# Optimization experiments

Measured on AMD Instinct MI355X. Metric: run time of the kernel, lower is better.

Reference implementation:

```python
import jax, jax.numpy as jnp
import numpy as np

H, C = 3, 64  # heads, per-head channels
NEG_SLOPE = 0.2

def setup_inputs() -> dict:
    key = jax.random.key(0)
    ks = jax.random.split(key, 8)
    B, N, D, E = 2, 50000, 128, 800000
    h = jax.random.normal(ks[0], (B, N, D), dtype=jnp.float32)
    edge_index = jax.random.randint(ks[1], (2, E), 0, N, dtype=jnp.int64)
    s = 1.0 / np.sqrt(D)
    W = jax.random.normal(ks[2], (D, H * C), dtype=jnp.float32) * s
    a_src = jax.random.normal(ks[3], (H, C), dtype=jnp.float32) * (1.0 / np.sqrt(C))
    a_dst = jax.random.normal(ks[4], (H, C), dtype=jnp.float32) * (1.0 / np.sqrt(C))
    bias = jnp.zeros((H * C,), dtype=jnp.float32)
    Wo = jax.random.normal(ks[5], (H * C, 1), dtype=jnp.float32) * (1.0 / np.sqrt(H * C))
    bo = jnp.zeros((1,), dtype=jnp.float32)
    return {"h": h, "edge_index": edge_index, "W": W, "a_src": a_src,
            "a_dst": a_dst, "bias": bias, "Wo": Wo, "bo": bo}

def _gat_single(h_b, src, dst, N, W, a_src, a_dst, bias):
    # h_b: [N, D] -> x: [N, H, C]
    x = (h_b @ W).reshape(-1, H, C)
    alpha_s = jnp.einsum('nhc,hc->nh', x, a_src)  # [N, H]
    alpha_d = jnp.einsum('nhc,hc->nh', x, a_dst)  # [N, H]
    e = alpha_s[src] + alpha_d[dst]               # [E', H]
    e = jnp.where(e > 0, e, NEG_SLOPE * e)        # leaky_relu(0.2)
    # segment softmax over edges grouped by destination node
    emax = jax.ops.segment_max(e, dst, num_segments=N)          # [N, H]
    p = jnp.exp(e - emax[dst])
    denom = jax.ops.segment_sum(p, dst, num_segments=N)         # [N, H]
    att = p / (denom[dst] + 1e-16)                               # [E', H]
    out = jax.ops.segment_sum(att[:, :, None] * x[src], dst, num_segments=N)  # [N,H,C]
    return out.reshape(-1, H * C) + bias

def reference(h, edge_index, W, a_src, a_dst, bias, Wo, bo):
    B, N, D = h.shape
    # PyG GATConv default: add self loops
    loops = jnp.arange(N, dtype=edge_index.dtype)
    src = jnp.concatenate([edge_index[0], loops])
    dst = jnp.concatenate([edge_index[1], loops])
    gat = jax.vmap(lambda hb: _gat_single(hb, src, dst, N, W, a_src, a_dst, bias))(h)
    gat = jax.nn.elu(gat)            # [B, N, H*C]; dropout inactive (eval)
    logits = gat @ Wo + bo           # [B, N, 1]
    return logits
```

## Files before the change

kernel.cpp:

```cpp
#include <hip/hip_runtime.h>
#include <hip/hip_bf16.h>
#include <math.h>

typedef __hip_bfloat16 bf16;
typedef __attribute__((ext_vector_type(8))) short short8;
typedef __attribute__((ext_vector_type(4))) float f32x4;

#define HC 192
#define DIN 128
#define NEG_SLOPE 0.2f
#define LCH 128
#define GN 4

static inline int cdiv(int a, int b){ return (a + b - 1) / b; }

__device__ inline short f2bf(float f){
  __hip_bfloat16 b = __float2bfloat16(f);
  return __builtin_bit_cast(short, b);
}
__device__ inline float loadf(const void* p, size_t i, int fm){
  return fm ? __bfloat162float(((const bf16*)p)[i]) : ((const float*)p)[i];
}
__device__ inline int eload(const void* p, long long i, int em){
  return em ? (int)(((const long long*)p)[i]) : ((const int*)p)[i];
}
__device__ inline unsigned pack2h(float a, float b){
  unsigned short ha = __builtin_bit_cast(unsigned short, (_Float16)a);
  unsigned short hb = __builtin_bit_cast(unsigned short, (_Float16)b);
  return (unsigned)ha | ((unsigned)hb << 16);
}
__device__ inline float unph(unsigned w, int hi){
  unsigned short hs = hi ? (unsigned short)(w >> 16) : (unsigned short)(w & 0xffff);
  return (float)__builtin_bit_cast(_Float16, hs);
}

__device__ inline int detect_fm(const unsigned* __restrict__ hw){
  unsigned w = hw[threadIdx.x & 63];
  unsigned expo = (w >> 7) & 0xFF;
  unsigned long long m = __ballot(expo >= 100 && expo <= 135);
  return __popcll(m) > 32;
}
__device__ inline int detect_em(const unsigned* __restrict__ ew){
  unsigned long long m = __ballot(ew[2*(threadIdx.x & 63) + 1] != 0);
  return __popcll(m) < 32;
}

__global__ void k_repack(const void* __restrict__ W, const void* __restrict__ a_src,
    const void* __restrict__ a_dst, const void* __restrict__ bias,
    const void* __restrict__ Wo, const void* __restrict__ bo,
    const unsigned* __restrict__ hw, bf16* __restrict__ Wt,
    float* __restrict__ asf, float* __restrict__ adf, float* __restrict__ biasf,
    float* __restrict__ Wof, float* __restrict__ bof){
  int fm = detect_fm(hw);
  int idx = blockIdx.x * 256 + threadIdx.x;
  if (idx < DIN * HC){
    int d = idx / HC, j = idx - d * HC;
    Wt[j * DIN + d] = __float2bfloat16(loadf(W, idx, fm));
  }
  if (idx < HC){
    asf[idx]   = loadf(a_src, idx, fm);
    adf[idx]   = loadf(a_dst, idx, fm);
    biasf[idx] = loadf(bias, idx, fm);
    Wof[idx]   = loadf(Wo, idx, fm);
  }
  if (idx == 0) bof[0] = loadf(bo, 0, fm);
}

__global__ __launch_bounds__(256) void k_gemm(const void* __restrict__ h,
    const bf16* __restrict__ Wt, bf16* __restrict__ x,
    const float* __restrict__ asf, const float* __restrict__ adf,
    float* __restrict__ asp, float* __restrict__ adp, int M, int N){
  int fm   = detect_fm((const unsigned*)h);
  int tid  = threadIdx.x;
  int w    = tid >> 6;
  int lane = tid & 63;
  int r16  = lane & 15;
  int quad = lane >> 4;
  __shared__ short ldsW[HC * 136];
  for (int c = tid; c < HC * 16; c += 256){
    int row = c >> 4, kg = c & 15;
    *(short8*)&ldsW[row * 136 + kg * 8] = *(const short8*)(Wt + row * DIN + kg * 8);
  }
  __syncthreads();

  int row  = blockIdx.x * 64 + w * 16 + r16;
  int lrow = min(row, M - 1);
  f32x4 acc[12];
  #pragma unroll
  for (int i = 0; i < 12; i++) acc[i] = (f32x4){0.f,0.f,0.f,0.f};
  size_t abase = (size_t)lrow * DIN + quad * 8;
  #pragma unroll
  for (int kb = 0; kb < 4; kb++){
    short8 af;
    if (fm == 0){
      const float* hf = (const float*)h + abase + kb * 32;
      float4 a = *(const float4*)hf;
      float4 b = *(const float4*)(hf + 4);
      af[0]=f2bf(a.x); af[1]=f2bf(a.y); af[2]=f2bf(a.z); af[3]=f2bf(a.w);
      af[4]=f2bf(b.x); af[5]=f2bf(b.y); af[6]=f2bf(b.z); af[7]=f2bf(b.w);
    } else {
      af = *(const short8*)((const bf16*)h + abase + kb * 32);
    }
    #pragma unroll
    for (int nt = 0; nt < 12; nt++){
      short8 bf_ = *(const short8*)&ldsW[(nt*16 + r16) * 136 + kb * 32 + quad * 8];
      acc[nt] = __builtin_amdgcn_mfma_f32_16x16x32_bf16(af, bf_, acc[nt], 0,0,0);
    }
  }
  int rbase = blockIdx.x * 64 + w * 16 + quad * 4;
  #pragma unroll
  for (int nt = 0; nt < 12; nt++){
    #pragma unroll
    for (int r = 0; r < 4; r++){
      int rr = rbase + r;
      if (rr < M) x[(size_t)rr * HC + nt*16 + r16] = __float2bfloat16(acc[nt][r]);
    }
  }
  float asv[12], adv[12];
  #pragma unroll
  for (int nt = 0; nt < 12; nt++){
    int col = (nt >> 2) * 64 + (nt & 3) * 16 + r16;
    asv[nt] = asf[col];
    adv[nt] = adf[col];
  }
  #pragma unroll
  for (int hh = 0; hh < 3; hh++){
    #pragma unroll
    for (int r = 0; r < 4; r++){
      float vs = acc[4*hh+0][r]*asv[4*hh+0] + acc[4*hh+1][r]*asv[4*hh+1]
               + acc[4*hh+2][r]*asv[4*hh+2] + acc[4*hh+3][r]*asv[4*hh+3];
      float vd = acc[4*hh+0][r]*adv[4*hh+0] + acc[4*hh+1][r]*adv[4*hh+1]
               + acc[4*hh+2][r]*adv[4*hh+2] + acc[4*hh+3][r]*adv[4*hh+3];
      #pragma unroll
      for (int off = 8; off; off >>= 1){
        vs += __shfl_down(vs, off, 16);
        vd += __shfl_down(vd, off, 16);
      }
      if (r16 == 0){
        int rr = rbase + r;
        if (rr < M){
          int b = rr >= N;
          int node = rr - b * N;
          asp[(size_t)node*8 + b*3 + hh] = vs;
          adp[(size_t)node*8 + b*3 + hh] = vd;
        }
      }
    }
  }
}

__global__ void k_hist(const void* __restrict__ ei, int E, int N, int* counts){
  int em = detect_em((const unsigned*)ei);
  int idx = blockIdx.x * 256 + threadIdx.x;
  if (idx >= E + N) return;
  int d = (idx < E) ? eload(ei, (long long)E + idx, em) : (idx - E);
  if ((unsigned)d < (unsigned)N) atomicAdd(&counts[d], 1);
}

__global__ __launch_bounds__(256) void k_scanA(const int* __restrict__ counts,
    int* __restrict__ partial, int* __restrict__ bsums, int N){
  __shared__ int s[256];
  int t = threadIdx.x, idx = blockIdx.x * 256 + t;
  int v = (idx < N) ? counts[idx] : 0;
  s[t] = v; __syncthreads();
  for (int o = 1; o < 256; o <<= 1){
    int u = (t >= o) ? s[t - o] : 0;
    __syncthreads();
    s[t] += u;
    __syncthreads();
  }
  if (idx < N) partial[idx] = s[t] - v;
  if (t == 255) bsums[blockIdx.x] = s[255];
}

__global__ __launch_bounds__(256) void k_scanC(const int* __restrict__ partial,
    const int* __restrict__ bsums, int* __restrict__ row_ptr,
    int* __restrict__ cursor, int N, int nb){
  __shared__ int s[256];
  int t = threadIdx.x;
  int v = (t < nb) ? bsums[t] : 0;
  s[t] = v; __syncthreads();
  for (int o = 1; o < 256; o <<= 1){
    int u = (t >= o) ? s[t - o] : 0;
    __syncthreads();
    s[t] += u;
    __syncthreads();
  }
  int excl = s[t] - v;
  __syncthreads();
  s[t] = excl;
  __syncthreads();
  int idx = blockIdx.x * 256 + t;
  int boff = s[blockIdx.x];
  if (idx < N){
    int val = partial[idx] + boff;
    row_ptr[idx] = val;
    cursor[idx]  = val;
  } else if (idx == N){
    row_ptr[N] = s[nb-1] + bsums[nb-1];
  }
}

__global__ void k_scatter(const void* __restrict__ ei, int E, int N,
    int* cursor, int2* __restrict__ esd){
  int em = detect_em((const unsigned*)ei);
  int idx = blockIdx.x * 256 + threadIdx.x;
  if (idx >= E + N) return;
  int s, d;
  if (idx < E){
    s = eload(ei, idx, em);
    d = eload(ei, (long long)E + idx, em);
  } else { s = d = idx - E; }
  if ((unsigned)d >= (unsigned)N) return;
  if ((unsigned)s >= (unsigned)N) s = 0;
  int p = atomicAdd(&cursor[d], 1);
  esd[p] = make_int2(s, d);
}

__global__ __launch_bounds__(256) void k_pe(const int2* __restrict__ esd,
    const float* __restrict__ asp, const float* __restrict__ adp,
    uint4* __restrict__ pe, int Etot){
  int j = blockIdx.x * 256 + threadIdx.x;
  if (j >= Etot) return;
  int2 sd = esd[j];
  float4 A0 = ((const float4*)asp)[(size_t)sd.x*2];
  float4 A1 = ((const float4*)asp)[(size_t)sd.x*2 + 1];
  float4 D0 = ((const float4*)adp)[(size_t)sd.y*2];
  float4 D1 = ((const float4*)adp)[(size_t)sd.y*2 + 1];
  float e0 = A0.x + D0.x, e1 = A0.y + D0.y, e2 = A0.z + D0.z;
  float e3 = A0.w + D0.w, e4 = A1.x + D1.x, e5 = A1.y + D1.y;
  e0 = e0 > 0.f ? e0 : NEG_SLOPE*e0;  e1 = e1 > 0.f ? e1 : NEG_SLOPE*e1;
  e2 = e2 > 0.f ? e2 : NEG_SLOPE*e2;  e3 = e3 > 0.f ? e3 : NEG_SLOPE*e3;
  e4 = e4 > 0.f ? e4 : NEG_SLOPE*e4;  e5 = e5 > 0.f ? e5 : NEG_SLOPE*e5;
  uint4 rec;
  rec.x = pack2h(__expf(e0), __expf(e1));
  rec.y = pack2h(__expf(e2), __expf(e3));
  rec.z = pack2h(__expf(e4), __expf(e5));
  rec.w = (unsigned)sd.x;
  pe[j] = rec;
}

__global__ __launch_bounds__(192) void k_gat(const bf16* __restrict__ x,
    const uint4* __restrict__ pe, const int* __restrict__ row_ptr,
    const float* __restrict__ biasf, const float* __restrict__ Wof,
    const float* __restrict__ bof, float* __restrict__ out, int N){
  int blk  = blockIdx.x;
  int t    = threadIdx.x;
  int node = t / 48;
  int u    = t - node * 48;
  int b    = u >= 24;
  int c8   = u - b * 24;
  int hh   = c8 >> 3;
  __shared__ int   rp[GN + 1];
  __shared__ uint4 ldsR[LCH];
  __shared__ float red[192];
  if (t < GN + 1) rp[t] = row_ptr[GN*blk + t];
  __syncthreads();
  int start = rp[node], end = rp[node + 1];
  int base0 = rp[0], cend = rp[GN];
  const ushort* xb = (const ushort*)x + (size_t)b * N * HC + c8 * 8;
  int pidx = b*3 + hh;
  int pw_i = pidx >> 1, pw_h = pidx & 1;
  unsigned* ldsU = (unsigned*)ldsR;
  float acc[8];
  #pragma unroll
  for (int k = 0; k < 8; k++) acc[k] = 0.f;
  float den = 0.f;
  for (int cb = base0; cb < cend; cb += LCH){
    int cnt = min(LCH, cend - cb);
    __syncthreads();
    for (int j = t; j < cnt; j += 192) ldsR[j] = pe[(size_t)cb + j];
    __syncthreads();
    int i0 = max(start, cb), i1 = min(end, cb + cnt);
    #pragma unroll 4
    for (int i = i0; i < i1; i++){
      int rec = i - cb;
      float p = unph(ldsU[rec*4 + pw_i], pw_h);
      int s   = (int)ldsU[rec*4 + 3];
      uint4 q = *(const uint4*)(xb + (size_t)s * HC);
      den += p;
      acc[0] = fmaf(p, __uint_as_float(q.x << 16),         acc[0]);
      acc[1] = fmaf(p, __uint_as_float(q.x & 0xffff0000u), acc[1]);
      acc[2] = fmaf(p, __uint_as_float(q.y << 16),         acc[2]);
      acc[3] = fmaf(p, __uint_as_float(q.y & 0xffff0000u), acc[3]);
      acc[4] = fmaf(p, __uint_as_float(q.z << 16),         acc[4]);
      acc[5] = fmaf(p, __uint_as_float(q.z & 0xffff0000u), acc[5]);
      acc[6] = fmaf(p, __uint_as_float(q.w << 16),         acc[6]);
      acc[7] = fmaf(p, __uint_as_float(q.w & 0xffff0000u), acc[7]);
    }
  }
  float inv = 1.f / (den + 1e-16f);
  float4 bi0 = ((const float4*)biasf)[c8*2], bi1 = ((const float4*)biasf)[c8*2+1];
  float4 w0  = ((const float4*)Wof)[c8*2],  w1  = ((const float4*)Wof)[c8*2+1];
  float r = 0.f;
  {
    float v;
    v = acc[0]*inv + bi0.x; v = v > 0.f ? v : expm1f(v); r += v * w0.x;
    v = acc[1]*inv + bi0.y; v = v > 0.f ? v : expm1f(v); r += v * w0.y;
    v = acc[2]*inv + bi0.z; v = v > 0.f ? v : expm1f(v); r += v * w0.z;
    v = acc[3]*inv + bi0.w; v = v > 0.f ? v : expm1f(v); r += v * w0.w;
    v = acc[4]*inv + bi1.x; v = v > 0.f ? v : expm1f(v); r += v * w1.x;
    v = acc[5]*inv + bi1.y; v = v > 0.f ? v : expm1f(v); r += v * w1.y;
    v = acc[6]*inv + bi1.z; v = v > 0.f ? v : expm1f(v); r += v * w1.z;
    v = acc[7]*inv + bi1.w; v = v > 0.f ? v : expm1f(v); r += v * w1.w;
  }
  red[t] = r;
  __syncthreads();
  if (t < 64){
    int g = t >> 3, l = t & 7;
    float v = red[g*24 + l] + red[g*24 + 8 + l] + red[g*24 + 16 + l];
    v += __shfl_down(v, 4, 8);
    v += __shfl_down(v, 2, 8);
    v += __shfl_down(v, 1, 8);
    if (l == 0){
      int nd = GN*blk + (g >> 1);
      int bb = g & 1;
      out[(size_t)bb * N + nd] = v + bof[0];
    }
  }
}

extern "C" void kernel_launch(void* const* d_in, const int* in_sizes, int n_in,
                              void* d_out, int out_size, void* d_ws, size_t ws_size,
                              hipStream_t stream){
  const void* h     = d_in[0];
  const void* ei    = d_in[1];
  const void* W     = d_in[2];
  const void* a_src = d_in[3];
  const void* a_dst = d_in[4];
  const void* bias  = d_in[5];
  const void* Wo    = d_in[6];
  const void* bo    = d_in[7];
  float* out = (float*)d_out;

  const int M    = in_sizes[0] / DIN;
  const int N    = M / 2;
  const int E    = in_sizes[1] / 2;
  const int Etot = E + N;

  char* ws = (char*)d_ws;
  size_t off = 0;
  auto alloc = [&](size_t bytes) -> void* {
    void* p = ws + off;
    off = (off + bytes + 511) & ~(size_t)511;
    return p;
  };
  bf16*  x       = (bf16*) alloc((size_t)M * HC * sizeof(bf16));
  float* asp     = (float*)alloc((size_t)N * 8 * sizeof(float));
  float* adp     = (float*)alloc((size_t)N * 8 * sizeof(float));
  int*   counts  = (int*)  alloc((size_t)N * sizeof(int));
  int*   partial = (int*)  alloc((size_t)N * sizeof(int));
  int*   row_ptr = (int*)  alloc((size_t)(N + 1) * sizeof(int));
  int*   cursor  = (int*)  alloc((size_t)N * sizeof(int));
  int*   bsums   = (int*)  alloc(256 * sizeof(int));
  int2*  esd     = (int2*) alloc((size_t)Etot * sizeof(int2));
  uint4* pe      = (uint4*)alloc((size_t)Etot * sizeof(uint4));
  bf16*  Wt      = (bf16*) alloc((size_t)DIN * HC * sizeof(bf16));
  float* asf     = (float*)alloc(HC * sizeof(float));
  float* adf     = (float*)alloc(HC * sizeof(float));
  float* biasf   = (float*)alloc(HC * sizeof(float));
  float* Wof     = (float*)alloc(HC * sizeof(float));
  float* bof     = (float*)alloc(16 * sizeof(float));
  (void)ws_size; (void)n_in; (void)out_size;

  hipMemsetAsync(counts, 0, (size_t)N * sizeof(int), stream);

  k_repack<<<cdiv(DIN * HC, 256), 256, 0, stream>>>(W, a_src, a_dst, bias, Wo, bo,
      (const unsigned*)h, Wt, asf, adf, biasf, Wof, bof);
  k_gemm<<<cdiv(M, 64), 256, 0, stream>>>(h, Wt, x, asf, adf, asp, adp, M, N);
  k_hist<<<cdiv(Etot, 256), 256, 0, stream>>>(ei, E, N, counts);
  int nb = cdiv(N, 256);
  k_scanA<<<nb, 256, 0, stream>>>(counts, partial, bsums, N);
  k_scanC<<<cdiv(N + 1, 256), 256, 0, stream>>>(partial, bsums, row_ptr, cursor, N, nb);
  k_scatter<<<cdiv(Etot, 256), 256, 0, stream>>>(ei, E, N, cursor, esd);
  k_pe<<<cdiv(Etot, 256), 256, 0, stream>>>(esd, asp, adp, pe, Etot);
  k_gat<<<N / GN, 192, 0, stream>>>(x, pe, row_ptr, biasf, Wof, bof, out, N);
}
```

Measured before the change: 315.1 us.

## Fuse CSR build and edge precompute into one persistent kernel with grid barriers

Replaces the histogram, two scan kernels, scatter and per-edge exp kernels with a single persistent kernel of 256 blocks that uses software grid barriers between phases. The scatter phase now computes the packed attention exponentials directly and writes them to the CSR slot, which removes the intermediate src/dst buffer and its extra write and read pass. This cuts four kernel launches and one global round trip. In exchange it relies on all 256 blocks being co-resident for the spin barriers, and it runs the edge loops with fewer threads using grid-stride loops. The single-block scan of block sums assumes at most 256 blocks, which fits N=50000.

```diff
diff --git a/kernel.cpp b/kernel.cpp
--- a/kernel.cpp
+++ b/kernel.cpp
@@ -11,6 +11,7 @@
 #define NEG_SLOPE 0.2f
 #define LCH 128
 #define GN 4
+#define CSRG 256
 
 static inline int cdiv(int a, int b){ return (a + b - 1) / b; }
 
@@ -43,6 +44,17 @@
 __device__ inline int detect_em(const unsigned* __restrict__ ew){
   unsigned long long m = __ballot(ew[2*(threadIdx.x & 63) + 1] != 0);
   return __popcll(m) < 32;
+}
+
+__device__ inline void gbar(int* bar, int id){
+  __syncthreads();
+  if (threadIdx.x == 0){
+    __threadfence();
+    __hip_atomic_fetch_add(&bar[id], 1, __ATOMIC_RELEASE, __HIP_MEMORY_SCOPE_AGENT);
+    while (__hip_atomic_load(&bar[id], __ATOMIC_ACQUIRE, __HIP_MEMORY_SCOPE_AGENT) < CSRG) {}
+    __threadfence();
+  }
+  __syncthreads();
 }
 
 __global__ void k_repack(const void* __restrict__ W, const void* __restrict__ a_src,
@@ -149,19 +161,24 @@
   }
 }
 
-__global__ void k_hist(const void* __restrict__ ei, int E, int N, int* counts){
+__global__ __launch_bounds__(256) void k_csr(const void* __restrict__ ei,
+    int E, int N, int* __restrict__ counts, int* __restrict__ bar,
+    int* __restrict__ partial, int* __restrict__ bsums,
+    int* __restrict__ row_ptr, int* __restrict__ cursor,
+    const float* __restrict__ asp, const float* __restrict__ adp,
+    uint4* __restrict__ pe){
   int em = detect_em((const unsigned*)ei);
-  int idx = blockIdx.x * 256 + threadIdx.x;
-  if (idx >= E + N) return;
-  int d = (idx < E) ? eload(ei, (long long)E + idx, em) : (idx - E);
-  if ((unsigned)d < (unsigned)N) atomicAdd(&counts[d], 1);
-}
-
-__global__ __launch_bounds__(256) void k_scanA(const int* __restrict__ counts,
-    int* __restrict__ partial, int* __restrict__ bsums, int N){
+  int t = threadIdx.x, blk = blockIdx.x;
+  int gt = blk * 256 + t;
+  const int GT = CSRG * 256;
+  int Etot = E + N;
+  for (int idx = gt; idx < Etot; idx += GT){
+    int d = (idx < E) ? eload(ei, (long long)E + idx, em) : (idx - E);
+    if ((unsigned)d < (unsigned)N) atomicAdd(&counts[d], 1);
+  }
+  gbar(bar, 0);
   __shared__ int s[256];
-  int t = threadIdx.x, idx = blockIdx.x * 256 + t;
-  int v = (idx < N) ? counts[idx] : 0;
+  int v = (gt < N) ? counts[gt] : 0;
   s[t] = v; __syncthreads();
   for (int o = 1; o < 256; o <<= 1){
     int u = (t >= o) ? s[t - o] : 0;
@@ -169,75 +186,52 @@
     s[t] += u;
     __syncthreads();
   }
-  if (idx < N) partial[idx] = s[t] - v;
-  if (t == 255) bsums[blockIdx.x] = s[255];
-}
-
-__global__ __launch_bounds__(256) void k_scanC(const int* __restrict__ partial,
-    const int* __restrict__ bsums, int* __restrict__ row_ptr,
-    int* __restrict__ cursor, int N, int nb){
-  __shared__ int s[256];
-  int t = threadIdx.x;
-  int v = (t < nb) ? bsums[t] : 0;
-  s[t] = v; __syncthreads();
+  if (gt < N) partial[gt] = s[t] - v;
+  if (t == 255) bsums[blk] = s[255];
+  gbar(bar, 1);
+  int v2 = bsums[t];
+  s[t] = v2; __syncthreads();
   for (int o = 1; o < 256; o <<= 1){
     int u = (t >= o) ? s[t - o] : 0;
     __syncthreads();
     s[t] += u;
     __syncthreads();
   }
-  int excl = s[t] - v;
-  __syncthreads();
-  s[t] = excl;
-  __syncthreads();
-  int idx = blockIdx.x * 256 + t;
-  int boff = s[blockIdx.x];
-  if (idx < N){
-    int val = partial[idx] + boff;
-    row_ptr[idx] = val;
-    cursor[idx]  = val;
-  } else if (idx == N){
-    row_ptr[N] = s[nb-1] + bsums[nb-1];
-  }
-}
-
-__global__ void k_scatter(const void* __restrict__ ei, int E, int N,
-    int* cursor, int2* __restrict__ esd){
-  int em = detect_em((const unsigned*)ei);
-  int idx = blockIdx.x * 256 + threadIdx.x;
-  if (idx >= E + N) return;
-  int s, d;
-  if (idx < E){
-    s = eload(ei, idx, em);
-    d = eload(ei, (long long)E + idx, em);
-  } else { s = d = idx - E; }
-  if ((unsigned)d >= (unsigned)N) return;
-  if ((unsigned)s >= (unsigned)N) s = 0;
-  int p = atomicAdd(&cursor[d], 1);
-  esd[p] = make_int2(s, d);
-}
-
-__global__ __launch_bounds__(256) void k_pe(const int2* __restrict__ esd,
-    const float* __restrict__ asp, const float* __restrict__ adp,
-    uint4* __restrict__ pe, int Etot){
-  int j = blockIdx.x * 256 + threadIdx.x;
-  if (j >= Etot) return;
-  int2 sd = esd[j];
-  float4 A0 = ((const float4*)asp)[(size_t)sd.x*2];
-  float4 A1 = ((const float4*)asp)[(size_t)sd.x*2 + 1];
-  float4 D0 = ((const float4*)adp)[(size_t)sd.y*2];
-  float4 D1 = ((const float4*)adp)[(size_t)sd.y*2 + 1];
-  float e0 = A0.x + D0.x, e1 = A0.y + D0.y, e2 = A0.z + D0.z;
-  float e3 = A0.w + D0.w, e4 = A1.x + D1.x, e5 = A1.y + D1.y;
-  e0 = e0 > 0.f ? e0 : NEG_SLOPE*e0;  e1 = e1 > 0.f ? e1 : NEG_SLOPE*e1;
-  e2 = e2 > 0.f ? e2 : NEG_SLOPE*e2;  e3 = e3 > 0.f ? e3 : NEG_SLOPE*e3;
-  e4 = e4 > 0.f ? e4 : NEG_SLOPE*e4;  e5 = e5 > 0.f ? e5 : NEG_SLOPE*e5;
-  uint4 rec;
-  rec.x = pack2h(__expf(e0), __expf(e1));
-  rec.y = pack2h(__expf(e2), __expf(e3));
-  rec.z = pack2h(__expf(e4), __expf(e5));
-  rec.w = (unsigned)sd.x;
-  pe[j] = rec;
+  int total = s[255];
+  int boff  = s[blk] - bsums[blk];
+  if (gt < N){
+    int val = partial[gt] + boff;
+    row_ptr[gt] = val;
+    cursor[gt]  = val;
+  } else if (gt == N){
+    row_ptr[N] = total;
+  }
+  gbar(bar, 2);
+  for (int idx = gt; idx < Etot; idx += GT){
+    int sn, d;
+    if (idx < E){
+      sn = eload(ei, idx, em);
+      d  = eload(ei, (long long)E + idx, em);
+    } else { sn = d = idx - E; }
+    if ((unsigned)d >= (unsigned)N) continue;
+    if ((unsigned)sn >= (unsigned)N) sn = 0;
+    int p = atomicAdd(&cursor[d], 1);
+    float4 A0 = ((const float4*)asp)[(size_t)sn*2];
+    float4 A1 = ((const float4*)asp)[(size_t)sn*2 + 1];
+    float4 D0 = ((const float4*)adp)[(size_t)d*2];
+    float4 D1 = ((const float4*)adp)[(size_t)d*2 + 1];
+    float e0 = A0.x + D0.x, e1 = A0.y + D0.y, e2 = A0.z + D0.z;
+    float e3 = A0.w + D0.w, e4 = A1.x + D1.x, e5 = A1.y + D1.y;
+    e0 = e0 > 0.f ? e0 : NEG_SLOPE*e0;  e1 = e1 > 0.f ? e1 : NEG_SLOPE*e1;
+    e2 = e2 > 0.f ? e2 : NEG_SLOPE*e2;  e3 = e3 > 0.f ? e3 : NEG_SLOPE*e3;
+    e4 = e4 > 0.f ? e4 : NEG_SLOPE*e4;  e5 = e5 > 0.f ? e5 : NEG_SLOPE*e5;
+    uint4 rec;
+    rec.x = pack2h(__expf(e0), __expf(e1));
+    rec.y = pack2h(__expf(e2), __expf(e3));
+    rec.z = pack2h(__expf(e4), __expf(e5));
+    rec.w = (unsigned)sn;
+    pe[p] = rec;
+  }
 }
 
 __global__ __launch_bounds__(192) void k_gat(const bf16* __restrict__ x,
@@ -348,12 +342,12 @@
   bf16*  x       = (bf16*) alloc((size_t)M * HC * sizeof(bf16));
   float* asp     = (float*)alloc((size_t)N * 8 * sizeof(float));
   float* adp     = (float*)alloc((size_t)N * 8 * sizeof(float));
-  int*   counts  = (int*)  alloc((size_t)N * sizeof(int));
+  int*   counts  = (int*)  alloc((size_t)(N + 16) * sizeof(int));
+  int*   bar     = counts + N;
   int*   partial = (int*)  alloc((size_t)N * sizeof(int));
   int*   row_ptr = (int*)  alloc((size_t)(N + 1) * sizeof(int));
   int*   cursor  = (int*)  alloc((size_t)N * sizeof(int));
   int*   bsums   = (int*)  alloc(256 * sizeof(int));
-  int2*  esd     = (int2*) alloc((size_t)Etot * sizeof(int2));
   uint4* pe      = (uint4*)alloc((size_t)Etot * sizeof(uint4));
   bf16*  Wt      = (bf16*) alloc((size_t)DIN * HC * sizeof(bf16));
   float* asf     = (float*)alloc(HC * sizeof(float));
@@ -363,16 +357,12 @@
   float* bof     = (float*)alloc(16 * sizeof(float));
   (void)ws_size; (void)n_in; (void)out_size;
 
-  hipMemsetAsync(counts, 0, (size_t)N * sizeof(int), stream);
+  hipMemsetAsync(counts, 0, (size_t)(N + 16) * sizeof(int), stream);
 
   k_repack<<<cdiv(DIN * HC, 256), 256, 0, stream>>>(W, a_src, a_dst, bias, Wo, bo,
       (const unsigned*)h, Wt, asf, adf, biasf, Wof, bof);
   k_gemm<<<cdiv(M, 64), 256, 0, stream>>>(h, Wt, x, asf, adf, asp, adp, M, N);
-  k_hist<<<cdiv(Etot, 256), 256, 0, stream>>>(ei, E, N, counts);
-  int nb = cdiv(N, 256);
-  k_scanA<<<nb, 256, 0, stream>>>(counts, partial, bsums, N);
-  k_scanC<<<cdiv(N + 1, 256), 256, 0, stream>>>(partial, bsums, row_ptr, cursor, N, nb);
-  k_scatter<<<cdiv(Etot, 256), 256, 0, stream>>>(ei, E, N, cursor, esd);
-  k_pe<<<cdiv(Etot, 256), 256, 0, stream>>>(esd, asp, adp, pe, Etot);
+  k_csr<<<CSRG, 256, 0, stream>>>(ei, E, N, counts, bar, partial, bsums,
+      row_ptr, cursor, asp, adp, pe);
   k_gat<<<N / GN, 192, 0, stream>>>(x, pe, row_ptr, biasf, Wof, bof, out, N);
 }
```

Result: slower. 364.9 us (+15.8%).
